# Kernel optimization log

Measured on AMD Instinct MI355X. Metric: run time of the kernel, lower is better.

## Reference

```python
import jax, jax.numpy as jnp
import numpy as np

B, C, L, D = 8, 16, 512, 256  # batch, channels (attended axis), seq len, d_model


def setup_inputs() -> dict:
    key = jax.random.key(0)
    ks = jax.random.split(key, 9)
    d = D
    x = jax.random.normal(ks[0], (B, C, L, D), dtype=jnp.float32)
    # qkv projection: Linear(d, 3d), xavier_normal weight, zero-ish bias
    Wqkv = jax.random.normal(ks[1], (3 * d, d), dtype=jnp.float32) * (2.0 / (4 * d)) ** 0.5
    bqkv = jnp.zeros((3 * d,), dtype=jnp.float32)
    # additive-attention scorer V: Linear(d, 1)
    Vw = jax.random.normal(ks[2], (1, d), dtype=jnp.float32) * (1.0 / d) ** 0.5
    Vb = jnp.zeros((1,), dtype=jnp.float32)
    bh = jnp.zeros((d,), dtype=jnp.float32)  # nn.Parameter(torch.zeros(d_model))
    ba = jnp.zeros((1,), dtype=jnp.float32)  # nn.Parameter(torch.zeros(1))
    # output projection Linear(d, d)
    Wout = jax.random.normal(ks[3], (d, d), dtype=jnp.float32) * (1.0 / d) ** 0.5
    bout = jnp.zeros((d,), dtype=jnp.float32)
    return {"x": x, "Wqkv": Wqkv, "bqkv": bqkv, "Vw": Vw, "Vb": Vb,
            "bh": bh, "ba": ba, "Wout": Wout, "bout": bout}


def reference(x, Wqkv, bqkv, Vw, Vb, bh, ba, Wout, bout):
    b, c, l, d = x.shape
    # (b, c, l, d) -> (b*l, c, d): attention over the channel axis c per position
    xf = jnp.transpose(x, (0, 2, 1, 3)).reshape(b * l, c, d)
    qkv = xf @ Wqkv.T + bqkv                       # (B, c, 3d)
    q, k, v = jnp.split(qkv, 3, axis=-1)           # each (B, c, d)
    # additive (Bahdanau) score: V(tanh(q_i + k_j + bh)) + ba
    h = jnp.tanh(q[:, :, None, :] + k[:, None, :, :] + bh)  # (B, c, c, d)
    score = jnp.einsum('bqkd,d->bqk', h, Vw[0]) + Vb[0] + ba[0]  # (B, c, c)
    A = jax.nn.softmax(score, axis=-1)             # stable softmax (matches exp(s-max)/sum)
    # torch einsum 'b c c, b c d -> b c d': repeated index -> DIAGONAL of A scales v
    z = jnp.einsum('bcc,bcd->bcd', A, v)           # (B, c, d)
    z = z.reshape(b, l, c, d).transpose(0, 2, 1, 3)  # (b, c, l, d)
    return z @ Wout.T + bout
```

## Files before the change

kernel.cpp:

```cpp
#include <hip/hip_runtime.h>


typedef __attribute__((ext_vector_type(8))) short bf16x8;
typedef __attribute__((ext_vector_type(4))) float f32x4;
typedef __attribute__((ext_vector_type(8))) _Float16 h16x8;
typedef __attribute__((ext_vector_type(4))) _Float16 h16x4;
typedef const __attribute__((address_space(1))) void* gp1_t;
typedef __attribute__((address_space(3))) void* lp3_t;

__device__ __forceinline__ unsigned short f2bf(float f) {
  union { float f; unsigned int u; } v; v.f = f;
  return (unsigned short)((v.u + 0x7FFFu + ((v.u >> 16) & 1u)) >> 16);
}

__global__ __launch_bounds__(256) void ca_prep_kernel(
    const float* __restrict__ Wqkv, const float* __restrict__ Wout,
    const float* __restrict__ bqkv,
    unsigned short* __restrict__ Wqb_t, unsigned short* __restrict__ Wcb_t,
    float* __restrict__ bcomb) {
  const int blk = blockIdx.x;
  if (blk < 64) {
    const int t = blk * 256 + threadIdx.x;
    const int k8 = t >> 9, n = t & 511;
    const float* src = Wqkv + (size_t)n * 256 + k8 * 8;
    const float4 v0 = *(const float4*)src;
    const float4 v1 = *(const float4*)(src + 4);
    bf16x8 o;
    o[0] = (short)f2bf(v0.x); o[1] = (short)f2bf(v0.y);
    o[2] = (short)f2bf(v0.z); o[3] = (short)f2bf(v0.w);
    o[4] = (short)f2bf(v1.x); o[5] = (short)f2bf(v1.y);
    o[6] = (short)f2bf(v1.z); o[7] = (short)f2bf(v1.w);
    *(bf16x8*)(Wqb_t + (size_t)t * 8) = o;
    return;
  }
  const int dp = blk - 64;
  const int e = threadIdx.x;
  const float* wrow = Wout + (size_t)dp * 256;
  float acc = 0.f;
  for (int f = 0; f < 256; ++f)
    acc = fmaf(wrow[f], Wqkv[(size_t)(512 + f) * 256 + e], acc);
  Wcb_t[((size_t)(e >> 3) * 256 + dp) * 8 + (e & 7)] = f2bf(acc);
  if (e == 0) {
    float b = 0.f;
    for (int f = 0; f < 256; ++f) b = fmaf(wrow[f], bqkv[512 + f], b);
    bcomb[dp] = b;
  }
}

__global__ __launch_bounds__(512, 6) void ca_fused(
    const float* __restrict__ x,
    const unsigned short* __restrict__ Wqb_t,
    const unsigned short* __restrict__ Wcb_t,
    const float* __restrict__ bqkv, const float* __restrict__ bh,
    const float* __restrict__ Vw,
    const float* __restrict__ bcomb, const float* __restrict__ bout,
    float* __restrict__ out) {
  __shared__ __align__(16) unsigned short xs[32 * 264];
  __shared__ __align__(16) unsigned short BsEs[16640];
  __shared__ __align__(16) float vw_s[256];
  __shared__ float af_s[32];
  unsigned short* const Bs = BsEs;
  _Float16* const Es = (_Float16*)BsEs;

  const int tid = threadIdx.x;
  const int lane = tid & 63, wave = tid >> 6;
  const int quad = lane >> 4, l15 = lane & 15;
  const int rt0 = blockIdx.x * 32;

  if (tid < 256) vw_s[tid] = -2.f * Vw[tid];

#pragma unroll
  for (int i = 0; i < 4; ++i) {
    const int sb = wave * 256 + i * 64;
    const unsigned short* g = Wqb_t + (size_t)(sb + lane) * 8;
    __builtin_amdgcn_global_load_lds((gp1_t)g, (lp3_t)(Bs + sb * 8), 16, 0, 0);
  }

  {
    const int rl = tid >> 4, c0 = (tid & 15) * 16;
    const int r = rt0 + rl;
    const int b = r >> 13, l = (r >> 4) & 511, c = r & 15;
    const float* src = x + ((size_t)(b * 16 + c) * 512 + l) * 256 + c0;
    unsigned short* dst = xs + rl * 264 + c0;
#pragma unroll
    for (int j = 0; j < 2; ++j) {
      const float4 v0 = *(const float4*)(src + j * 8);
      const float4 v1 = *(const float4*)(src + j * 8 + 4);
      bf16x8 o;
      o[0] = (short)f2bf(v0.x); o[1] = (short)f2bf(v0.y);
      o[2] = (short)f2bf(v0.z); o[3] = (short)f2bf(v0.w);
      o[4] = (short)f2bf(v1.x); o[5] = (short)f2bf(v1.y);
      o[6] = (short)f2bf(v1.z); o[7] = (short)f2bf(v1.w);
      *(bf16x8*)(dst + j * 8) = o;
    }
  }
  __syncthreads();

  f32x4 acc[2][4] = {};
  for (int k0c = 0; k0c < 8; ++k0c) {
    bf16x8 af[2], bfr[4];
#pragma unroll
    for (int mi = 0; mi < 2; ++mi)
      af[mi] = *(const bf16x8*)&xs[(mi * 16 + l15) * 264 + k0c * 32 + quad * 8];
#pragma unroll
    for (int ni = 0; ni < 4; ++ni)
      bfr[ni] = *(const bf16x8*)&Bs[(quad * 512 + wave * 64 + ni * 16 + l15) * 8];
    __syncthreads();
    if (k0c < 7) {
#pragma unroll
      for (int i = 0; i < 4; ++i) {
        const int sb = wave * 256 + i * 64;
        const unsigned short* g =
            Wqb_t + ((size_t)(k0c + 1) * 2048 + sb + lane) * 8;
        __builtin_amdgcn_global_load_lds((gp1_t)g, (lp3_t)(Bs + sb * 8), 16, 0, 0);
      }
    }
#pragma unroll
    for (int mi = 0; mi < 2; ++mi)
#pragma unroll
      for (int ni = 0; ni < 4; ++ni)
        acc[mi][ni] = __builtin_amdgcn_mfma_f32_16x16x32_bf16(
            bfr[ni], af[mi], acc[mi][ni], 0, 0, 0);
    __syncthreads();
  }

  const float SC = 2.8853900817779268f;
  const bool isq = (wave < 4);
#pragma unroll
  for (int mi = 0; mi < 2; ++mi) {
    const int rl = mi * 16 + l15;
#pragma unroll
    for (int ni = 0; ni < 4; ++ni) {
      const int n = wave * 64 + ni * 16 + quad * 4;
      const float4 bq = *(const float4*)(bqkv + n);
      float4 bhv = make_float4(0.f, 0.f, 0.f, 0.f);
      if (isq) bhv = *(const float4*)(bh + n);
      h16x4 st;
      st[0] = (_Float16)__builtin_amdgcn_exp2f(
          fminf(15.f, fmaxf(-15.f, (acc[mi][ni][0] + bq.x + bhv.x) * SC)));
      st[1] = (_Float16)__builtin_amdgcn_exp2f(
          fminf(15.f, fmaxf(-15.f, (acc[mi][ni][1] + bq.y + bhv.y) * SC)));
      st[2] = (_Float16)__builtin_amdgcn_exp2f(
          fminf(15.f, fmaxf(-15.f, (acc[mi][ni][2] + bq.z + bhv.z) * SC)));
      st[3] = (_Float16)__builtin_amdgcn_exp2f(
          fminf(15.f, fmaxf(-15.f, (acc[mi][ni][3] + bq.w + bhv.w) * SC)));
      *(h16x4*)&Es[rl * 520 + n] = st;
    }
  }
  __syncthreads();

  {
    const int p = tid >> 8, qc = (tid >> 4) & 15, kc = tid & 15;
    const _Float16* eqp = Es + (p * 16 + qc) * 520;
    const _Float16* ekp = Es + (p * 16 + kc) * 520 + 256;
    f32x4 a4 = {};
#pragma unroll 4
    for (int d = 0; d < 256; d += 8) {
      const h16x8 eq = *(const h16x8*)(eqp + d);
      const h16x8 ek = *(const h16x8*)(ekp + d);
      const f32x4 wv0 = *(const f32x4*)(vw_s + d);
      const f32x4 wv1 = *(const f32x4*)(vw_s + d + 4);
      f32x4 sg0, sg1;
      sg0.x = __builtin_amdgcn_rcpf(1.f + (float)eq[0] * (float)ek[0]);
      sg0.y = __builtin_amdgcn_rcpf(1.f + (float)eq[1] * (float)ek[1]);
      sg0.z = __builtin_amdgcn_rcpf(1.f + (float)eq[2] * (float)ek[2]);
      sg0.w = __builtin_amdgcn_rcpf(1.f + (float)eq[3] * (float)ek[3]);
      sg1.x = __builtin_amdgcn_rcpf(1.f + (float)eq[4] * (float)ek[4]);
      sg1.y = __builtin_amdgcn_rcpf(1.f + (float)eq[5] * (float)ek[5]);
      sg1.z = __builtin_amdgcn_rcpf(1.f + (float)eq[6] * (float)ek[6]);
      sg1.w = __builtin_amdgcn_rcpf(1.f + (float)eq[7] * (float)ek[7]);
      a4 += wv0 * sg0 + wv1 * sg1;
    }
    float s = (a4[0] + a4[1]) + (a4[2] + a4[3]);
    float m = s;
    for (int off = 8; off; off >>= 1) m = fmaxf(m, __shfl_xor(m, off, 16));
    const float e = __builtin_amdgcn_exp2f((s - m) * 1.4426950408889634f);
    float sum = e;
    for (int off = 8; off; off >>= 1) sum += __shfl_xor(sum, off, 16);
    if (kc == qc) af_s[p * 16 + qc] = e / sum;
  }
  __syncthreads();

#pragma unroll
  for (int i = 0; i < 2; ++i) {
    const int sb = wave * 128 + i * 64;
    const unsigned short* g = Wcb_t + (size_t)(sb + lane) * 8;
    __builtin_amdgcn_global_load_lds((gp1_t)g, (lp3_t)(Bs + sb * 8), 16, 0, 0);
  }
  __syncthreads();

  f32x4 acc2[2][2] = {};
  for (int k0c = 0; k0c < 8; ++k0c) {
    bf16x8 af[2], bfr[2];
#pragma unroll
    for (int mi = 0; mi < 2; ++mi)
      af[mi] = *(const bf16x8*)&xs[(mi * 16 + l15) * 264 + k0c * 32 + quad * 8];
#pragma unroll
    for (int ni = 0; ni < 2; ++ni)
      bfr[ni] = *(const bf16x8*)&Bs[(quad * 256 + wave * 32 + ni * 16 + l15) * 8];
    __syncthreads();
    if (k0c < 7) {
#pragma unroll
      for (int i = 0; i < 2; ++i) {
        const int sb = wave * 128 + i * 64;
        const unsigned short* g =
            Wcb_t + ((size_t)(k0c + 1) * 1024 + sb + lane) * 8;
        __builtin_amdgcn_global_load_lds((gp1_t)g, (lp3_t)(Bs + sb * 8), 16, 0, 0);
      }
    }
#pragma unroll
    for (int mi = 0; mi < 2; ++mi)
#pragma unroll
      for (int ni = 0; ni < 2; ++ni)
        acc2[mi][ni] = __builtin_amdgcn_mfma_f32_16x16x32_bf16(
            bfr[ni], af[mi], acc2[mi][ni], 0, 0, 0);
    __syncthreads();
  }

#pragma unroll
  for (int mi = 0; mi < 2; ++mi) {
    const int rl = mi * 16 + l15;
    const int r = rt0 + rl;
    const int c = r & 15, p = r >> 4;
    const int l = p & 511, b = p >> 9;
    const float av = af_s[rl];
    float* orow = out + ((size_t)(b * 16 + c) * 512 + l) * 256;
#pragma unroll
    for (int ni = 0; ni < 2; ++ni) {
      const int n = wave * 32 + ni * 16 + quad * 4;
      const float4 bc = *(const float4*)(bcomb + n);
      const float4 bo = *(const float4*)(bout + n);
      float4 o;
      o.x = fmaf(av, acc2[mi][ni][0] + bc.x, bo.x);
      o.y = fmaf(av, acc2[mi][ni][1] + bc.y, bo.y);
      o.z = fmaf(av, acc2[mi][ni][2] + bc.z, bo.z);
      o.w = fmaf(av, acc2[mi][ni][3] + bc.w, bo.w);
      *(float4*)(orow + n) = o;
    }
  }
}

extern "C" void kernel_launch(void* const* d_in, const int* in_sizes, int n_in,
                              void* d_out, int out_size, void* d_ws, size_t ws_size,
                              hipStream_t stream) {
  (void)in_sizes; (void)n_in; (void)out_size; (void)ws_size;
  const float* x    = (const float*)d_in[0];
  const float* Wqkv = (const float*)d_in[1];
  const float* bqkv = (const float*)d_in[2];
  const float* Vw   = (const float*)d_in[3];
  const float* bh   = (const float*)d_in[5];
  const float* Wout = (const float*)d_in[7];
  const float* bout = (const float*)d_in[8];
  float* out = (float*)d_out;

  float* bcomb = (float*)d_ws;
  unsigned short* Wqb_t = (unsigned short*)(bcomb + 256);
  unsigned short* Wcb_t = Wqb_t + (size_t)512 * 256;

  ca_prep_kernel<<<dim3(320), dim3(256), 0, stream>>>(
      Wqkv, Wout, bqkv, Wqb_t, Wcb_t, bcomb);
  ca_fused<<<dim3(2048), dim3(512), 0, stream>>>(
      x, Wqb_t, Wcb_t, bqkv, bh, Vw, bcomb, bout, out);
}
```

Baseline: 195.8 us.

## Load GEMM weight fragments directly from global into registers, drop LDS staging

Both GEMM phases now read their bf16 weight fragments straight from global memory into registers, double-buffered one k-chunk ahead. Before, they were staged into shared memory with global_load_lds and a pair of block-wide barriers per k-chunk. This removes about 32 __syncthreads and the LDS round trip for weights, and it lets the output-projection GEMM start without an extra barrier. In exchange, every wave re-reads weights from L2/global with more register pressure, and the shared Es buffer is no longer aliased with the weight staging area.

```diff
diff --git a/kernel.cpp b/kernel.cpp
--- a/kernel.cpp
+++ b/kernel.cpp
@@ -5,8 +5,6 @@
 typedef __attribute__((ext_vector_type(4))) float f32x4;
 typedef __attribute__((ext_vector_type(8))) _Float16 h16x8;
 typedef __attribute__((ext_vector_type(4))) _Float16 h16x4;
-typedef const __attribute__((address_space(1))) void* gp1_t;
-typedef __attribute__((address_space(3))) void* lp3_t;
 
 __device__ __forceinline__ unsigned short f2bf(float f) {
   union { float f; unsigned int u; } v; v.f = f;
@@ -56,11 +54,9 @@
     const float* __restrict__ bcomb, const float* __restrict__ bout,
     float* __restrict__ out) {
   __shared__ __align__(16) unsigned short xs[32 * 264];
-  __shared__ __align__(16) unsigned short BsEs[16640];
+  __shared__ __align__(16) _Float16 Es[32 * 520];
   __shared__ __align__(16) float vw_s[256];
   __shared__ float af_s[32];
-  unsigned short* const Bs = BsEs;
-  _Float16* const Es = (_Float16*)BsEs;
 
   const int tid = threadIdx.x;
   const int lane = tid & 63, wave = tid >> 6;
@@ -68,13 +64,6 @@
   const int rt0 = blockIdx.x * 32;
 
   if (tid < 256) vw_s[tid] = -2.f * Vw[tid];
-
-#pragma unroll
-  for (int i = 0; i < 4; ++i) {
-    const int sb = wave * 256 + i * 64;
-    const unsigned short* g = Wqb_t + (size_t)(sb + lane) * 8;
-    __builtin_amdgcn_global_load_lds((gp1_t)g, (lp3_t)(Bs + sb * 8), 16, 0, 0);
-  }
 
   {
     const int rl = tid >> 4, c0 = (tid & 15) * 16;
@@ -97,31 +86,34 @@
   __syncthreads();
 
   f32x4 acc[2][4] = {};
-  for (int k0c = 0; k0c < 8; ++k0c) {
-    bf16x8 af[2], bfr[4];
-#pragma unroll
-    for (int mi = 0; mi < 2; ++mi)
-      af[mi] = *(const bf16x8*)&xs[(mi * 16 + l15) * 264 + k0c * 32 + quad * 8];
+  {
+    const unsigned short* b1 = Wqb_t + quad * 4096 + (wave * 64 + l15) * 8;
+    bf16x8 bcur[4], bnxt[4];
 #pragma unroll
     for (int ni = 0; ni < 4; ++ni)
-      bfr[ni] = *(const bf16x8*)&Bs[(quad * 512 + wave * 64 + ni * 16 + l15) * 8];
-    __syncthreads();
-    if (k0c < 7) {
-#pragma unroll
-      for (int i = 0; i < 4; ++i) {
-        const int sb = wave * 256 + i * 64;
-        const unsigned short* g =
-            Wqb_t + ((size_t)(k0c + 1) * 2048 + sb + lane) * 8;
-        __builtin_amdgcn_global_load_lds((gp1_t)g, (lp3_t)(Bs + sb * 8), 16, 0, 0);
-      }
-    }
-#pragma unroll
-    for (int mi = 0; mi < 2; ++mi)
-#pragma unroll
-      for (int ni = 0; ni < 4; ++ni)
-        acc[mi][ni] = __builtin_amdgcn_mfma_f32_16x16x32_bf16(
-            bfr[ni], af[mi], acc[mi][ni], 0, 0, 0);
-    __syncthreads();
+      bcur[ni] = *(const bf16x8*)(b1 + ni * 128);
+#pragma unroll
+    for (int c = 0; c < 8; ++c) {
+      if (c < 7) {
+#pragma unroll
+        for (int ni = 0; ni < 4; ++ni)
+          bnxt[ni] = *(const bf16x8*)(b1 + (size_t)(c + 1) * 16384 + ni * 128);
+      }
+      bf16x8 af[2];
+#pragma unroll
+      for (int mi = 0; mi < 2; ++mi)
+        af[mi] = *(const bf16x8*)&xs[(mi * 16 + l15) * 264 + c * 32 + quad * 8];
+#pragma unroll
+      for (int mi = 0; mi < 2; ++mi)
+#pragma unroll
+        for (int ni = 0; ni < 4; ++ni)
+          acc[mi][ni] = __builtin_amdgcn_mfma_f32_16x16x32_bf16(
+              bcur[ni], af[mi], acc[mi][ni], 0, 0, 0);
+      if (c < 7) {
+#pragma unroll
+        for (int ni = 0; ni < 4; ++ni) bcur[ni] = bnxt[ni];
+      }
+    }
   }
 
   const float SC = 2.8853900817779268f;
@@ -179,43 +171,38 @@
     for (int off = 8; off; off >>= 1) sum += __shfl_xor(sum, off, 16);
     if (kc == qc) af_s[p * 16 + qc] = e / sum;
   }
+
+  f32x4 acc2[2][2] = {};
+  {
+    const unsigned short* b2 = Wcb_t + quad * 2048 + (wave * 32 + l15) * 8;
+    bf16x8 bcur[2], bnxt[2];
+#pragma unroll
+    for (int ni = 0; ni < 2; ++ni)
+      bcur[ni] = *(const bf16x8*)(b2 + ni * 128);
+#pragma unroll
+    for (int c = 0; c < 8; ++c) {
+      if (c < 7) {
+#pragma unroll
+        for (int ni = 0; ni < 2; ++ni)
+          bnxt[ni] = *(const bf16x8*)(b2 + (size_t)(c + 1) * 8192 + ni * 128);
+      }
+      bf16x8 af[2];
+#pragma unroll
+      for (int mi = 0; mi < 2; ++mi)
+        af[mi] = *(const bf16x8*)&xs[(mi * 16 + l15) * 264 + c * 32 + quad * 8];
+#pragma unroll
+      for (int mi = 0; mi < 2; ++mi)
+#pragma unroll
+        for (int ni = 0; ni < 2; ++ni)
+          acc2[mi][ni] = __builtin_amdgcn_mfma_f32_16x16x32_bf16(
+              bcur[ni], af[mi], acc2[mi][ni], 0, 0, 0);
+      if (c < 7) {
+#pragma unroll
+        for (int ni = 0; ni < 2; ++ni) bcur[ni] = bnxt[ni];
+      }
+    }
+  }
   __syncthreads();
-
-#pragma unroll
-  for (int i = 0; i < 2; ++i) {
-    const int sb = wave * 128 + i * 64;
-    const unsigned short* g = Wcb_t + (size_t)(sb + lane) * 8;
-    __builtin_amdgcn_global_load_lds((gp1_t)g, (lp3_t)(Bs + sb * 8), 16, 0, 0);
-  }
-  __syncthreads();
-
-  f32x4 acc2[2][2] = {};
-  for (int k0c = 0; k0c < 8; ++k0c) {
-    bf16x8 af[2], bfr[2];
-#pragma unroll
-    for (int mi = 0; mi < 2; ++mi)
-      af[mi] = *(const bf16x8*)&xs[(mi * 16 + l15) * 264 + k0c * 32 + quad * 8];
-#pragma unroll
-    for (int ni = 0; ni < 2; ++ni)
-      bfr[ni] = *(const bf16x8*)&Bs[(quad * 256 + wave * 32 + ni * 16 + l15) * 8];
-    __syncthreads();
-    if (k0c < 7) {
-#pragma unroll
-      for (int i = 0; i < 2; ++i) {
-        const int sb = wave * 128 + i * 64;
-        const unsigned short* g =
-            Wcb_t + ((size_t)(k0c + 1) * 1024 + sb + lane) * 8;
-        __builtin_amdgcn_global_load_lds((gp1_t)g, (lp3_t)(Bs + sb * 8), 16, 0, 0);
-      }
-    }
-#pragma unroll
-    for (int mi = 0; mi < 2; ++mi)
-#pragma unroll
-      for (int ni = 0; ni < 2; ++ni)
-        acc2[mi][ni] = __builtin_amdgcn_mfma_f32_16x16x32_bf16(
-            bfr[ni], af[mi], acc2[mi][ni], 0, 0, 0);
-    __syncthreads();
-  }
 
 #pragma unroll
   for (int mi = 0; mi < 2; ++mi) {
```

Measured after the change: 203.2 us. 1.04x slower.

## Interleave output-projection MFMAs with additive-score VALU loop; use packed bf16 convert

Applied to the files above, without the earlier changes.

The second GEMM (x times the combined output weight) now runs inside the additive score loop. Its B fragments are loaded straight from global memory into registers with one-step prefetch, replacing the LDS staging and its per-chunk barriers. This lets the matrix-core work overlap the rcp-heavy VALU score computation and removes the separate GEMM phase with its syncs. The x-to-bf16 conversion also switches to the hardware v_cvt_pk_bf16_f32 instruction. The cost is more register pressure and uncoalesced direct global loads of the weights per wave.

```diff
diff --git a/kernel.cpp b/kernel.cpp
--- a/kernel.cpp
+++ b/kernel.cpp
@@ -11,6 +11,12 @@
 __device__ __forceinline__ unsigned short f2bf(float f) {
   union { float f; unsigned int u; } v; v.f = f;
   return (unsigned short)((v.u + 0x7FFFu + ((v.u >> 16) & 1u)) >> 16);
+}
+
+__device__ __forceinline__ unsigned int cvt_pk_bf16(float a, float b) {
+  unsigned int r;
+  asm("v_cvt_pk_bf16_f32 %0, %1, %2" : "=v"(r) : "v"(a), "v"(b));
+  return r;
 }
 
 __global__ __launch_bounds__(256) void ca_prep_kernel(
@@ -86,12 +92,12 @@
     for (int j = 0; j < 2; ++j) {
       const float4 v0 = *(const float4*)(src + j * 8);
       const float4 v1 = *(const float4*)(src + j * 8 + 4);
-      bf16x8 o;
-      o[0] = (short)f2bf(v0.x); o[1] = (short)f2bf(v0.y);
-      o[2] = (short)f2bf(v0.z); o[3] = (short)f2bf(v0.w);
-      o[4] = (short)f2bf(v1.x); o[5] = (short)f2bf(v1.y);
-      o[6] = (short)f2bf(v1.z); o[7] = (short)f2bf(v1.w);
-      *(bf16x8*)(dst + j * 8) = o;
+      uint4 o;
+      o.x = cvt_pk_bf16(v0.x, v0.y);
+      o.y = cvt_pk_bf16(v0.z, v0.w);
+      o.z = cvt_pk_bf16(v1.x, v1.y);
+      o.w = cvt_pk_bf16(v1.z, v1.w);
+      *(uint4*)(dst + j * 8) = o;
     }
   }
   __syncthreads();
@@ -149,27 +155,47 @@
   }
   __syncthreads();
 
+  f32x4 acc2[2][2] = {};
   {
     const int p = tid >> 8, qc = (tid >> 4) & 15, kc = tid & 15;
     const _Float16* eqp = Es + (p * 16 + qc) * 520;
     const _Float16* ekp = Es + (p * 16 + kc) * 520 + 256;
+    const unsigned short* wb2 = Wcb_t + (size_t)(quad * 256 + wave * 32 + l15) * 8;
+    bf16x8 bcur0 = *(const bf16x8*)(wb2);
+    bf16x8 bcur1 = *(const bf16x8*)(wb2 + 128);
     f32x4 a4 = {};
-#pragma unroll 4
-    for (int d = 0; d < 256; d += 8) {
-      const h16x8 eq = *(const h16x8*)(eqp + d);
-      const h16x8 ek = *(const h16x8*)(ekp + d);
-      const f32x4 wv0 = *(const f32x4*)(vw_s + d);
-      const f32x4 wv1 = *(const f32x4*)(vw_s + d + 4);
-      f32x4 sg0, sg1;
-      sg0.x = __builtin_amdgcn_rcpf(1.f + (float)eq[0] * (float)ek[0]);
-      sg0.y = __builtin_amdgcn_rcpf(1.f + (float)eq[1] * (float)ek[1]);
-      sg0.z = __builtin_amdgcn_rcpf(1.f + (float)eq[2] * (float)ek[2]);
-      sg0.w = __builtin_amdgcn_rcpf(1.f + (float)eq[3] * (float)ek[3]);
-      sg1.x = __builtin_amdgcn_rcpf(1.f + (float)eq[4] * (float)ek[4]);
-      sg1.y = __builtin_amdgcn_rcpf(1.f + (float)eq[5] * (float)ek[5]);
-      sg1.z = __builtin_amdgcn_rcpf(1.f + (float)eq[6] * (float)ek[6]);
-      sg1.w = __builtin_amdgcn_rcpf(1.f + (float)eq[7] * (float)ek[7]);
-      a4 += wv0 * sg0 + wv1 * sg1;
+#pragma unroll
+    for (int c = 0; c < 8; ++c) {
+      bf16x8 bnxt0, bnxt1;
+      if (c < 7) {
+        bnxt0 = *(const bf16x8*)(wb2 + (size_t)(c + 1) * 8192);
+        bnxt1 = *(const bf16x8*)(wb2 + (size_t)(c + 1) * 8192 + 128);
+      }
+      bf16x8 af0 = *(const bf16x8*)&xs[l15 * 264 + c * 32 + quad * 8];
+      bf16x8 af1 = *(const bf16x8*)&xs[(16 + l15) * 264 + c * 32 + quad * 8];
+#pragma unroll
+      for (int j = 0; j < 4; ++j) {
+        const int d = c * 32 + j * 8;
+        const h16x8 eq = *(const h16x8*)(eqp + d);
+        const h16x8 ek = *(const h16x8*)(ekp + d);
+        const f32x4 wv0 = *(const f32x4*)(vw_s + d);
+        const f32x4 wv1 = *(const f32x4*)(vw_s + d + 4);
+        f32x4 sg0, sg1;
+        sg0.x = __builtin_amdgcn_rcpf(1.f + (float)eq[0] * (float)ek[0]);
+        sg0.y = __builtin_amdgcn_rcpf(1.f + (float)eq[1] * (float)ek[1]);
+        sg0.z = __builtin_amdgcn_rcpf(1.f + (float)eq[2] * (float)ek[2]);
+        sg0.w = __builtin_amdgcn_rcpf(1.f + (float)eq[3] * (float)ek[3]);
+        sg1.x = __builtin_amdgcn_rcpf(1.f + (float)eq[4] * (float)ek[4]);
+        sg1.y = __builtin_amdgcn_rcpf(1.f + (float)eq[5] * (float)ek[5]);
+        sg1.z = __builtin_amdgcn_rcpf(1.f + (float)eq[6] * (float)ek[6]);
+        sg1.w = __builtin_amdgcn_rcpf(1.f + (float)eq[7] * (float)ek[7]);
+        a4 += wv0 * sg0 + wv1 * sg1;
+      }
+      acc2[0][0] = __builtin_amdgcn_mfma_f32_16x16x32_bf16(bcur0, af0, acc2[0][0], 0, 0, 0);
+      acc2[0][1] = __builtin_amdgcn_mfma_f32_16x16x32_bf16(bcur1, af0, acc2[0][1], 0, 0, 0);
+      acc2[1][0] = __builtin_amdgcn_mfma_f32_16x16x32_bf16(bcur0, af1, acc2[1][0], 0, 0, 0);
+      acc2[1][1] = __builtin_amdgcn_mfma_f32_16x16x32_bf16(bcur1, af1, acc2[1][1], 0, 0, 0);
+      bcur0 = bnxt0; bcur1 = bnxt1;
     }
     float s = (a4[0] + a4[1]) + (a4[2] + a4[3]);
     float m = s;
@@ -180,42 +206,6 @@
     if (kc == qc) af_s[p * 16 + qc] = e / sum;
   }
   __syncthreads();
-
-#pragma unroll
-  for (int i = 0; i < 2; ++i) {
-    const int sb = wave * 128 + i * 64;
-    const unsigned short* g = Wcb_t + (size_t)(sb + lane) * 8;
-    __builtin_amdgcn_global_load_lds((gp1_t)g, (lp3_t)(Bs + sb * 8), 16, 0, 0);
-  }
-  __syncthreads();
-
-  f32x4 acc2[2][2] = {};
-  for (int k0c = 0; k0c < 8; ++k0c) {
-    bf16x8 af[2], bfr[2];
-#pragma unroll
-    for (int mi = 0; mi < 2; ++mi)
-      af[mi] = *(const bf16x8*)&xs[(mi * 16 + l15) * 264 + k0c * 32 + quad * 8];
-#pragma unroll
-    for (int ni = 0; ni < 2; ++ni)
-      bfr[ni] = *(const bf16x8*)&Bs[(quad * 256 + wave * 32 + ni * 16 + l15) * 8];
-    __syncthreads();
-    if (k0c < 7) {
-#pragma unroll
-      for (int i = 0; i < 2; ++i) {
-        const int sb = wave * 128 + i * 64;
-        const unsigned short* g =
-            Wcb_t + ((size_t)(k0c + 1) * 1024 + sb + lane) * 8;
-        __builtin_amdgcn_global_load_lds((gp1_t)g, (lp3_t)(Bs + sb * 8), 16, 0, 0);
-      }
-    }
-#pragma unroll
-    for (int mi = 0; mi < 2; ++mi)
-#pragma unroll
-      for (int ni = 0; ni < 2; ++ni)
-        acc2[mi][ni] = __builtin_amdgcn_mfma_f32_16x16x32_bf16(
-            bfr[ni], af[mi], acc2[mi][ni], 0, 0, 0);
-    __syncthreads();
-  }
 
 #pragma unroll
   for (int mi = 0; mi < 2; ++mi) {
```

Result: faster. 190.8 us (-2.6%).
